# Optimization experiments

Measured on AMD Instinct MI355X. Metric: run time of the kernel, lower is better.

The kernel has to match this reference:

```python
import jax, jax.numpy as jnp
import numpy as np
import math

D_MODEL = 1024
NUM_HEADS = 16
SEQ = 2048
BATCH = 2


def setup_inputs() -> dict:
    key = jax.random.key(0)
    ks = jax.random.split(key, 12)
    s = 1.0 / math.sqrt(D_MODEL)
    inp = {
        "query": jax.random.normal(ks[0], (SEQ, BATCH, D_MODEL), jnp.float32),
        "key": jax.random.normal(ks[1], (SEQ, BATCH, D_MODEL), jnp.float32),
        "value": jax.random.normal(ks[2], (SEQ, BATCH, D_MODEL), jnp.float32),
        "Wq": jax.random.normal(ks[3], (D_MODEL, D_MODEL), jnp.float32) * s,
        "bq": jax.random.normal(ks[4], (D_MODEL,), jnp.float32) * 0.01,
        "Wk": jax.random.normal(ks[5], (D_MODEL, D_MODEL), jnp.float32) * s,
        "bk": jax.random.normal(ks[6], (D_MODEL,), jnp.float32) * 0.01,
        "Wv": jax.random.normal(ks[7], (D_MODEL, D_MODEL), jnp.float32) * s,
        "bv": jax.random.normal(ks[8], (D_MODEL,), jnp.float32) * 0.01,
        "Wo": jax.random.normal(ks[9], (D_MODEL, D_MODEL), jnp.float32) * s,
        "bo": jax.random.normal(ks[10], (D_MODEL,), jnp.float32) * 0.01,
    }
    # causal (subsequent) mask: True above the diagonal means masked
    inp["attn_mask"] = jnp.triu(jnp.ones((SEQ, SEQ), bool), k=1)
    # key_padding_mask: True = padding; random lengths in [SEQ//2, SEQ]
    lengths = jax.random.randint(ks[11], (BATCH,), SEQ // 2, SEQ + 1)
    inp["key_padding_mask"] = jnp.arange(SEQ)[None, :] >= lengths[:, None]
    return inp


def reference(query, key, value, Wq, bq, Wk, bk, Wv, bv, Wo, bo, attn_mask, key_padding_mask):
    S, B, D = query.shape
    H = NUM_HEADS
    dk = D // H

    def proj_split(x, W, b):
        y = x @ W.T + b                      # [S, B, D]
        return y.reshape(S, B, H, dk).transpose(1, 2, 0, 3)  # [B, H, S, dk]

    q = proj_split(query, Wq, bq)
    k = proj_split(key, Wk, bk)
    v = proj_split(value, Wv, bv)

    scores = jnp.einsum("bhqd,bhkd->bhqk", q, k) / jnp.sqrt(jnp.float32(dk))
    mask = key_padding_mask[:, None, None, :] | attn_mask[None, None, :, :]
    scores = jnp.where(mask, -jnp.inf, scores)
    p = jax.nn.softmax(scores, axis=-1)       # [B, H, S, S]
    x = jnp.einsum("bhqk,bhkd->bhqd", p, v)   # [B, H, S, dk]
    x = x.transpose(2, 0, 1, 3).reshape(S, B, D)
    return x @ Wo.T + bo
```

## Files before the change

### kernel.cpp

```cpp
#include <hip/hip_runtime.h>
#include <hip/hip_bf16.h>

#define S_LEN 2048
#define BATCH 2
#define DMODEL 1024
#define NHEAD 16
#define DK 64

typedef __bf16 bf16_t;
typedef bf16_t bf16x4 __attribute__((ext_vector_type(4)));
typedef bf16_t bf16x8 __attribute__((ext_vector_type(8)));
typedef float floatx4 __attribute__((ext_vector_type(4)));

#define SEG  ((size_t)S_LEN * BATCH * DMODEL)
#define WSEG ((size_t)DMODEL * DMODEL)
#define CVT_TOT (3 * SEG + 4 * WSEG)
#define CVT_BLOCKS 4096

#define QSCALE 0.180336879f

__global__ void cvt_all(const float* __restrict__ q, const float* __restrict__ k,
                        const float* __restrict__ v, const float* __restrict__ wq,
                        const float* __restrict__ wk, const float* __restrict__ wv,
                        const float* __restrict__ wo, bf16_t* __restrict__ out,
                        const unsigned char* __restrict__ am,
                        const unsigned char* __restrict__ kpm,
                        int* __restrict__ lens)
{
    if (blockIdx.x >= CVT_BLOCKS) {
        const int b = (int)blockIdx.x - CVT_BLOCKS;
        __shared__ int cnt;
        const int t = threadIdx.x;
        if (t == 0) cnt = 0;
        int st;
        if (am[1]) st = 1;
        else if (am[2] | am[3]) st = 2;
        else st = 4;
        __syncthreads();
        int local = 0;
        for (int idx = t; idx < S_LEN; idx += blockDim.x) {
            int nz = 0;
            for (int c = 0; c < st; c++) nz |= kpm[(b * S_LEN + idx) * st + c];
            local += (nz != 0);
        }
        local += __shfl_xor(local, 1);  local += __shfl_xor(local, 2);
        local += __shfl_xor(local, 4);  local += __shfl_xor(local, 8);
        local += __shfl_xor(local, 16); local += __shfl_xor(local, 32);
        if ((t & 63) == 0) atomicAdd(&cnt, local);
        __syncthreads();
        if (t == 0) lens[b] = S_LEN - cnt;
        return;
    }

    size_t i4 = ((size_t)blockIdx.x * blockDim.x + threadIdx.x) * 4;
    const size_t stride = (size_t)CVT_BLOCKS * blockDim.x * 4;
    for (; i4 < CVT_TOT; i4 += stride) {
        const float* src;
        size_t off;
        if (i4 < SEG)                    { src = q;  off = i4; }
        else if (i4 < 2 * SEG)           { src = k;  off = i4 - SEG; }
        else if (i4 < 3 * SEG)           { src = v;  off = i4 - 2 * SEG; }
        else if (i4 < 3 * SEG + WSEG)    { src = wq; off = i4 - 3 * SEG; }
        else if (i4 < 3 * SEG + 2 * WSEG){ src = wk; off = i4 - (3 * SEG + WSEG); }
        else if (i4 < 3 * SEG + 3 * WSEG){ src = wv; off = i4 - (3 * SEG + 2 * WSEG); }
        else                             { src = wo; off = i4 - (3 * SEG + 3 * WSEG); }
        const float4 x = *(const float4*)(src + off);
        bf16x4 r;
        r[0] = (bf16_t)x.x; r[1] = (bf16_t)x.y; r[2] = (bf16_t)x.z; r[3] = (bf16_t)x.w;
        *(bf16x4*)(out + i4) = r;
    }
}

__global__ __launch_bounds__(256, 3)
void gemm_qkv(const bf16_t* __restrict__ Abase, const bf16_t* __restrict__ Wbase,
              const float* __restrict__ bq, const float* __restrict__ bk,
              const float* __restrict__ bv, bf16_t* __restrict__ Obase)
{
    __shared__ bf16_t As[128 * 32];
    __shared__ bf16_t Bs[128 * 32];

    const int L   = (int)(blockIdx.x + (blockIdx.y << 3) + (blockIdx.z << 8));
    const int xcd = L & 7;
    const int w   = L >> 3;
    const int z   = w >> 5;
    const int mBase = ((xcd << 2) | (w & 3)) * 128;
    const int nBase = ((w >> 2) & 7) * 128;

    const bf16_t* A = Abase + (size_t)z * SEG;
    const bf16_t* W = Wbase + (size_t)z * WSEG;
    const float* bias = (z == 0) ? bq : (z == 1) ? bk : bv;
    bf16_t* C = Obase + (size_t)z * SEG;

    const int t    = threadIdx.x;
    const int wave = t >> 6;
    const int lane = t & 63;
    const int l15  = lane & 15;
    const int quad = lane >> 4;

    const int wRow  = (wave >> 1) * 64;
    const int wCol  = (wave & 1) * 64;
    const int psw   = (l15 >> 1) & 3;

    floatx4 acc[4][4];
#pragma unroll
    for (int i = 0; i < 4; i++)
#pragma unroll
        for (int j = 0; j < 4; j++) acc[i][j] = (floatx4){0.f, 0.f, 0.f, 0.f};

    for (int k0 = 0; k0 < DMODEL; k0 += 32) {
#pragma unroll
        for (int c = 0; c < 2; c++) {
            const int chunk = c * 256 + t;
            const int row   = chunk >> 2;
            const int lc    = ((chunk & 3) ^ ((row >> 1) & 3)) * 8;
            const bf16_t* gA = A + (size_t)(mBase + row) * DMODEL + k0 + lc;
            const bf16_t* gB = W + (size_t)(nBase + row) * DMODEL + k0 + lc;
            bf16_t* lA = As + (c * 256 + wave * 64) * 8;
            bf16_t* lB = Bs + (c * 256 + wave * 64) * 8;
            __builtin_amdgcn_global_load_lds(
                (const __attribute__((address_space(1))) void*)gA,
                (__attribute__((address_space(3))) void*)lA, 16, 0, 0);
            __builtin_amdgcn_global_load_lds(
                (const __attribute__((address_space(1))) void*)gB,
                (__attribute__((address_space(3))) void*)lB, 16, 0, 0);
        }
        __syncthreads();

        bf16x8 af[4], bfr[4];
#pragma unroll
        for (int mi = 0; mi < 4; mi++)
            af[mi] = *(const bf16x8*)(As + (wRow + mi * 16 + l15) * 32
                                         + ((quad ^ psw)) * 8);
#pragma unroll
        for (int ni = 0; ni < 4; ni++)
            bfr[ni] = *(const bf16x8*)(Bs + (wCol + ni * 16 + l15) * 32
                                          + ((quad ^ psw)) * 8);
#pragma unroll
        for (int mi = 0; mi < 4; mi++)
#pragma unroll
            for (int ni = 0; ni < 4; ni++)
                acc[mi][ni] = __builtin_amdgcn_mfma_f32_16x16x32_bf16(
                    af[mi], bfr[ni], acc[mi][ni], 0, 0, 0);
        __syncthreads();
    }

    const float scale = (z == 0) ? QSCALE : 1.0f;
    float bvv[4];
#pragma unroll
    for (int ni = 0; ni < 4; ni++)
        bvv[ni] = bias[nBase + wCol + ni * 16 + l15];

#pragma unroll
    for (int mi = 0; mi < 4; mi++) {
#pragma unroll
        for (int ni = 0; ni < 4; ni++) {
            const int n = nBase + wCol + ni * 16 + l15;
            const int h = n >> 6, i = n & 63;
#pragma unroll
            for (int j = 0; j < 4; j++) {
                const int m = mBase + wRow + mi * 16 + quad * 4 + j;
                const int s = m >> 1, b = m & 1;
                const float v = (acc[mi][ni][j] + bvv[ni]) * scale;
                size_t off;
                if (z < 2)
                    off = ((size_t)(b * NHEAD + h) * S_LEN + s) * DK + i;
                else
                    off = ((size_t)(b * NHEAD + h) * DK + i) * S_LEN + s;
                C[off] = (bf16_t)v;
            }
        }
    }
}

__global__ __launch_bounds__(256, 4)
void attn(const bf16_t* __restrict__ qw, const bf16_t* __restrict__ kw,
          const bf16_t* __restrict__ vw, bf16_t* __restrict__ ow,
          const int* __restrict__ lens)
{
    __shared__ bf16_t Ks[2][64 * 64];
    __shared__ bf16_t Vs[2][64 * 64];
    __shared__ bf16_t Ps[4][16 * 64];

    const int t    = threadIdx.x;
    const int wave = t >> 6;
    const int lane = t & 63;
    const int l15  = lane & 15;
    const int quad = lane >> 4;
    const int qg   = lane & 48;
    const int rowbase = qg >> 2;

    const int n  = (int)(blockIdx.x + (blockIdx.y << 5));
    const int r  = n >> 8;
    const int j  = (n >> 3) & 31;
    const int bh = (n & 7) | (r << 3);
    const int flip  = (r == 1) | (r == 2);
    const int qTile = flip ? (31 - j) : j;
    const int b     = bh >> 4;
    const int len   = lens[b];
    const int qBase = qTile * 64;

    const bf16_t* kbase = kw + (size_t)bh * S_LEN * DK;
    const bf16_t* vbase = vw + (size_t)bh * DK * S_LEN;

    const int dr = lane >> 3;
    const int cc = (lane & 7) ^ dr;

    const bf16_t* Qg = qw + ((size_t)bh * S_LEN + qBase + wave * 16) * DK;
    const bf16x8 qa0 = *(const bf16x8*)(Qg + l15 * DK + quad * 8);
    const bf16x8 qa1 = *(const bf16x8*)(Qg + l15 * DK + 32 + quad * 8);

    floatx4 O[4];
#pragma unroll
    for (int i = 0; i < 4; i++) O[i] = (floatx4){0.f, 0.f, 0.f, 0.f};
    float lrow = 0.f;

    const int ktEnd = min(qTile, (len - 1) >> 6);

    auto dma_tile = [&](int ktB, int buf) {
#pragma unroll
        for (int i = 0; i < 2; i++) {
            const int R0 = (wave * 2 + i) * 8;
            const bf16_t* gK = kbase + (size_t)(ktB + R0 + dr) * DK + cc * 8;
            const bf16_t* gV = vbase + (size_t)(R0 + dr) * S_LEN + ktB + cc * 8;
            bf16_t* lK = &Ks[buf][(size_t)R0 * 64];
            bf16_t* lV = &Vs[buf][(size_t)R0 * 64];
            __builtin_amdgcn_global_load_lds(
                (const __attribute__((address_space(1))) void*)gK,
                (__attribute__((address_space(3))) void*)lK, 16, 0, 0);
            __builtin_amdgcn_global_load_lds(
                (const __attribute__((address_space(1))) void*)gV,
                (__attribute__((address_space(3))) void*)lV, 16, 0, 0);
        }
    };

    dma_tile(0, 0);
    __syncthreads();

    const int sw  = l15 & 7;
    const int ch0 = (quad ^ sw) * 8;
    const int ch1 = ((4 | quad) ^ sw) * 8;

    for (int kt = 0; kt <= ktEnd; kt++) {
        const int cur = kt & 1;
        if (kt < ktEnd) dma_tile((kt + 1) * 64, cur ^ 1);

        floatx4 sc[4];
#pragma unroll
        for (int ni = 0; ni < 4; ni++) {
            const bf16_t* kr = &Ks[cur][(ni * 16 + l15) * 64];
            const bf16x8 kf0 = *(const bf16x8*)(kr + ch0);
            const bf16x8 kf1 = *(const bf16x8*)(kr + ch1);
            floatx4 zz = (floatx4){0.f, 0.f, 0.f, 0.f};
            zz = __builtin_amdgcn_mfma_f32_16x16x32_bf16(kf0, qa0, zz, 0, 0, 0);
            zz = __builtin_amdgcn_mfma_f32_16x16x32_bf16(kf1, qa1, zz, 0, 0, 0);
            sc[ni] = zz;
        }

        const int ktBase = kt * 64;
        const int q = qBase + wave * 16 + l15;
        const bool needMask = (kt == qTile) || (ktBase + 64 > len);
        if (needMask) {
#pragma unroll
            for (int ni = 0; ni < 4; ni++) {
#pragma unroll
                for (int rr = 0; rr < 4; rr++) {
                    const int key = ktBase + ni * 16 + quad * 4 + rr;
                    if (key > q || key >= len) sc[ni][rr] = -3.0e38f;
                }
            }
        }

        float lsum = 0.f;
#pragma unroll
        for (int ni = 0; ni < 4; ni++) {
#pragma unroll
            for (int rr = 0; rr < 4; rr++) {
                const float p = exp2f(sc[ni][rr]);
                sc[ni][rr] = p;
                lsum += p;
            }
        }
        lrow += lsum;

        bf16_t* Pw = Ps[wave];
#pragma unroll
        for (int ni = 0; ni < 4; ni++) {
            bf16x4 pk;
            pk[0] = (bf16_t)sc[ni][0]; pk[1] = (bf16_t)sc[ni][1];
            pk[2] = (bf16_t)sc[ni][2]; pk[3] = (bf16_t)sc[ni][3];
            const int lc = 2 * ni + (quad >> 1);
            *(bf16x4*)(Pw + l15 * 64 + ((lc ^ sw) << 3) + (quad & 1) * 4) = pk;
        }

        const bf16x8 pa0 = *(const bf16x8*)(Pw + l15 * 64 + ((quad ^ sw) << 3));
        const bf16x8 pa1 = *(const bf16x8*)(Pw + l15 * 64 + (((4 | quad) ^ sw) << 3));
#pragma unroll
        for (int nd = 0; nd < 4; nd++) {
            const bf16_t* vr = &Vs[cur][(nd * 16 + l15) * 64];
            const bf16x8 vb0 = *(const bf16x8*)(vr + ch0);
            const bf16x8 vb1 = *(const bf16x8*)(vr + ch1);
            O[nd] = __builtin_amdgcn_mfma_f32_16x16x32_bf16(pa0, vb0, O[nd], 0, 0, 0);
            O[nd] = __builtin_amdgcn_mfma_f32_16x16x32_bf16(pa1, vb1, O[nd], 0, 0, 0);
        }
        __syncthreads();
    }

    lrow += __shfl_xor(lrow, 16);
    lrow += __shfl_xor(lrow, 32);

    float rinv[4];
#pragma unroll
    for (int jj = 0; jj < 4; jj++)
        rinv[jj] = 1.0f / __shfl(lrow, qg | (rowbase + jj));
#pragma unroll
    for (int nd = 0; nd < 4; nd++) {
        const int d = (bh & 15) * DK + nd * 16 + l15;
#pragma unroll
        for (int jj = 0; jj < 4; jj++) {
            const int qq = qBase + wave * 16 + quad * 4 + jj;
            ow[((size_t)qq * BATCH + b) * DMODEL + d] = (bf16_t)(O[nd][jj] * rinv[jj]);
        }
    }
}

__global__ __launch_bounds__(256, 2)
void gemm_o(const bf16_t* __restrict__ A, const bf16_t* __restrict__ W,
            const float* __restrict__ bias, float* __restrict__ C)
{
    __shared__ bf16_t As[128 * 32];
    __shared__ bf16_t Bs[64 * 32];

    const int L   = (int)(blockIdx.x + (blockIdx.y << 4));
    const int xcd = L & 7;
    const int w   = L >> 3;
    const int mBase = ((xcd << 2) | (w & 3)) * 128;
    const int nBase = (w >> 2) * 64;

    const int t    = threadIdx.x;
    const int wave = t >> 6;
    const int lane = t & 63;
    const int l15  = lane & 15;
    const int quad = lane >> 4;

    const int wRow  = wave * 32;
    const int psw   = (l15 >> 1) & 3;

    floatx4 acc[2][4];
#pragma unroll
    for (int i = 0; i < 2; i++)
#pragma unroll
        for (int j = 0; j < 4; j++) acc[i][j] = (floatx4){0.f, 0.f, 0.f, 0.f};

    for (int k0 = 0; k0 < DMODEL; k0 += 32) {
#pragma unroll
        for (int c = 0; c < 2; c++) {
            const int chunk = c * 256 + t;
            const int row   = chunk >> 2;
            const int lc    = ((chunk & 3) ^ ((row >> 1) & 3)) * 8;
            const bf16_t* gA = A + (size_t)(mBase + row) * DMODEL + k0 + lc;
            bf16_t* lA = As + (c * 256 + wave * 64) * 8;
            __builtin_amdgcn_global_load_lds(
                (const __attribute__((address_space(1))) void*)gA,
                (__attribute__((address_space(3))) void*)lA, 16, 0, 0);
        }
        {
            const int row = t >> 2;
            const int lc  = ((t & 3) ^ ((row >> 1) & 3)) * 8;
            const bf16_t* gB = W + (size_t)(nBase + row) * DMODEL + k0 + lc;
            bf16_t* lB = Bs + (wave * 64) * 8;
            __builtin_amdgcn_global_load_lds(
                (const __attribute__((address_space(1))) void*)gB,
                (__attribute__((address_space(3))) void*)lB, 16, 0, 0);
        }
        __syncthreads();

        bf16x8 af[2], bfr[4];
#pragma unroll
        for (int mi = 0; mi < 2; mi++)
            af[mi] = *(const bf16x8*)(As + (wRow + mi * 16 + l15) * 32
                                         + ((quad ^ psw)) * 8);
#pragma unroll
        for (int ni = 0; ni < 4; ni++)
            bfr[ni] = *(const bf16x8*)(Bs + (ni * 16 + l15) * 32
                                          + ((quad ^ psw)) * 8);
#pragma unroll
        for (int mi = 0; mi < 2; mi++)
#pragma unroll
            for (int ni = 0; ni < 4; ni++)
                acc[mi][ni] = __builtin_amdgcn_mfma_f32_16x16x32_bf16(
                    af[mi], bfr[ni], acc[mi][ni], 0, 0, 0);
        __syncthreads();
    }

    float bvv[4];
#pragma unroll
    for (int ni = 0; ni < 4; ni++)
        bvv[ni] = bias[nBase + ni * 16 + l15];

#pragma unroll
    for (int mi = 0; mi < 2; mi++) {
#pragma unroll
        for (int ni = 0; ni < 4; ni++) {
            const int n = nBase + ni * 16 + l15;
#pragma unroll
            for (int j = 0; j < 4; j++) {
                const int m = mBase + wRow + mi * 16 + quad * 4 + j;
                C[(size_t)m * DMODEL + n] = acc[mi][ni][j] + bvv[ni];
            }
        }
    }
}

extern "C" void kernel_launch(void* const* d_in, const int* in_sizes, int n_in,
                              void* d_out, int out_size, void* d_ws, size_t ws_size,
                              hipStream_t stream)
{
    const float* query = (const float*)d_in[0];
    const float* key   = (const float*)d_in[1];
    const float* value = (const float*)d_in[2];
    const float* Wq = (const float*)d_in[3];
    const float* bq = (const float*)d_in[4];
    const float* Wk = (const float*)d_in[5];
    const float* bk = (const float*)d_in[6];
    const float* Wv = (const float*)d_in[7];
    const float* bv = (const float*)d_in[8];
    const float* Wo = (const float*)d_in[9];
    const float* bo = (const float*)d_in[10];
    const unsigned char* am  = (const unsigned char*)d_in[11];
    const unsigned char* kpm = (const unsigned char*)d_in[12];

    bf16_t* cvt   = (bf16_t*)d_ws;
    bf16_t* q_bf  = cvt;
    bf16_t* wq_bf = cvt + 3 * SEG;
    bf16_t* wo_bf = wq_bf + 3 * WSEG;
    bf16_t* q_ws  = cvt + CVT_TOT;
    bf16_t* k_ws  = q_ws + SEG;
    bf16_t* v_ws  = k_ws + SEG;
    bf16_t* o_ws  = q_bf;
    int*    lens  = (int*)(v_ws + SEG);

    cvt_all<<<CVT_BLOCKS + BATCH, 256, 0, stream>>>(
        query, key, value, Wq, Wk, Wv, Wo, cvt, am, kpm, lens);

    gemm_qkv<<<dim3(DMODEL / 128, (S_LEN * BATCH) / 128, 3), dim3(256), 0, stream>>>(
        q_bf, wq_bf, bq, bk, bv, q_ws);

    attn<<<dim3(32, BATCH * NHEAD), dim3(256), 0, stream>>>(
        q_ws, k_ws, v_ws, o_ws, lens);

    gemm_o<<<dim3(DMODEL / 64, (S_LEN * BATCH) / 128), dim3(256), 0, stream>>>(
        o_ws, wo_bf, bo, (float*)d_out);
}
```

Baseline: 228.3 us.

## Double-buffer LDS tiles in QKV and output projection GEMMs

Both projection GEMMs now keep two shared-memory buffers for A and B tiles. Each iteration issues the global-to-LDS load for the next K-slice before reading the current slice and running the MFMAs, so global memory latency can overlap with compute. One barrier per iteration is removed. In exchange, shared memory per block doubles, which could limit how many blocks fit on a CU.

New measurement: 236.4 us. 1.04x slower.

```diff
diff --git a/kernel.cpp b/kernel.cpp
--- a/kernel.cpp
+++ b/kernel.cpp
@@ -76,8 +76,8 @@
               const float* __restrict__ bq, const float* __restrict__ bk,
               const float* __restrict__ bv, bf16_t* __restrict__ Obase)
 {
-    __shared__ bf16_t As[128 * 32];
-    __shared__ bf16_t Bs[128 * 32];
+    __shared__ bf16_t As[2][128 * 32];
+    __shared__ bf16_t Bs[2][128 * 32];
 
     const int L   = (int)(blockIdx.x + (blockIdx.y << 3) + (blockIdx.z << 8));
     const int xcd = L & 7;
@@ -107,7 +107,7 @@
 #pragma unroll
         for (int j = 0; j < 4; j++) acc[i][j] = (floatx4){0.f, 0.f, 0.f, 0.f};
 
-    for (int k0 = 0; k0 < DMODEL; k0 += 32) {
+    auto stage = [&](int k0, int buf) {
 #pragma unroll
         for (int c = 0; c < 2; c++) {
             const int chunk = c * 256 + t;
@@ -115,8 +115,8 @@
             const int lc    = ((chunk & 3) ^ ((row >> 1) & 3)) * 8;
             const bf16_t* gA = A + (size_t)(mBase + row) * DMODEL + k0 + lc;
             const bf16_t* gB = W + (size_t)(nBase + row) * DMODEL + k0 + lc;
-            bf16_t* lA = As + (c * 256 + wave * 64) * 8;
-            bf16_t* lB = Bs + (c * 256 + wave * 64) * 8;
+            bf16_t* lA = As[buf] + (c * 256 + wave * 64) * 8;
+            bf16_t* lB = Bs[buf] + (c * 256 + wave * 64) * 8;
             __builtin_amdgcn_global_load_lds(
                 (const __attribute__((address_space(1))) void*)gA,
                 (__attribute__((address_space(3))) void*)lA, 16, 0, 0);
@@ -124,17 +124,24 @@
                 (const __attribute__((address_space(1))) void*)gB,
                 (__attribute__((address_space(3))) void*)lB, 16, 0, 0);
         }
-        __syncthreads();
+    };
+
+    stage(0, 0);
+    __syncthreads();
+
+    for (int ks = 0; ks < DMODEL / 32; ks++) {
+        const int cur = ks & 1;
+        if (ks < DMODEL / 32 - 1) stage((ks + 1) * 32, cur ^ 1);
 
         bf16x8 af[4], bfr[4];
 #pragma unroll
         for (int mi = 0; mi < 4; mi++)
-            af[mi] = *(const bf16x8*)(As + (wRow + mi * 16 + l15) * 32
-                                         + ((quad ^ psw)) * 8);
+            af[mi] = *(const bf16x8*)(As[cur] + (wRow + mi * 16 + l15) * 32
+                                             + ((quad ^ psw)) * 8);
 #pragma unroll
         for (int ni = 0; ni < 4; ni++)
-            bfr[ni] = *(const bf16x8*)(Bs + (wCol + ni * 16 + l15) * 32
-                                          + ((quad ^ psw)) * 8);
+            bfr[ni] = *(const bf16x8*)(Bs[cur] + (wCol + ni * 16 + l15) * 32
+                                              + ((quad ^ psw)) * 8);
 #pragma unroll
         for (int mi = 0; mi < 4; mi++)
 #pragma unroll
@@ -327,8 +334,8 @@
 void gemm_o(const bf16_t* __restrict__ A, const bf16_t* __restrict__ W,
             const float* __restrict__ bias, float* __restrict__ C)
 {
-    __shared__ bf16_t As[128 * 32];
-    __shared__ bf16_t Bs[64 * 32];
+    __shared__ bf16_t As[2][128 * 32];
+    __shared__ bf16_t Bs[2][64 * 32];
 
     const int L   = (int)(blockIdx.x + (blockIdx.y << 4));
     const int xcd = L & 7;
@@ -351,14 +358,14 @@
 #pragma unroll
         for (int j = 0; j < 4; j++) acc[i][j] = (floatx4){0.f, 0.f, 0.f, 0.f};
 
-    for (int k0 = 0; k0 < DMODEL; k0 += 32) {
+    auto stage = [&](int k0, int buf) {
 #pragma unroll
         for (int c = 0; c < 2; c++) {
             const int chunk = c * 256 + t;
             const int row   = chunk >> 2;
             const int lc    = ((chunk & 3) ^ ((row >> 1) & 3)) * 8;
             const bf16_t* gA = A + (size_t)(mBase + row) * DMODEL + k0 + lc;
-            bf16_t* lA = As + (c * 256 + wave * 64) * 8;
+            bf16_t* lA = As[buf] + (c * 256 + wave * 64) * 8;
             __builtin_amdgcn_global_load_lds(
                 (const __attribute__((address_space(1))) void*)gA,
                 (__attribute__((address_space(3))) void*)lA, 16, 0, 0);
@@ -367,22 +374,29 @@
             const int row = t >> 2;
             const int lc  = ((t & 3) ^ ((row >> 1) & 3)) * 8;
             const bf16_t* gB = W + (size_t)(nBase + row) * DMODEL + k0 + lc;
-            bf16_t* lB = Bs + (wave * 64) * 8;
+            bf16_t* lB = Bs[buf] + (wave * 64) * 8;
             __builtin_amdgcn_global_load_lds(
                 (const __attribute__((address_space(1))) void*)gB,
                 (__attribute__((address_space(3))) void*)lB, 16, 0, 0);
         }
-        __syncthreads();
+    };
+
+    stage(0, 0);
+    __syncthreads();
+
+    for (int ks = 0; ks < DMODEL / 32; ks++) {
+        const int cur = ks & 1;
+        if (ks < DMODEL / 32 - 1) stage((ks + 1) * 32, cur ^ 1);
 
         bf16x8 af[2], bfr[4];
 #pragma unroll
         for (int mi = 0; mi < 2; mi++)
-            af[mi] = *(const bf16x8*)(As + (wRow + mi * 16 + l15) * 32
-                                         + ((quad ^ psw)) * 8);
+            af[mi] = *(const bf16x8*)(As[cur] + (wRow + mi * 16 + l15) * 32
+                                             + ((quad ^ psw)) * 8);
 #pragma unroll
         for (int ni = 0; ni < 4; ni++)
-            bfr[ni] = *(const bf16x8*)(Bs + (ni * 16 + l15) * 32
-                                          + ((quad ^ psw)) * 8);
+            bfr[ni] = *(const bf16x8*)(Bs[cur] + (ni * 16 + l15) * 32
+                                              + ((quad ^ psw)) * 8);
 #pragma unroll
         for (int mi = 0; mi < 2; mi++)
 #pragma unroll
```
